# Performance work log

Measured on AMD Instinct MI355X. Metric: run time of the kernel, lower is better.

Reference implementation:

```python
import jax, jax.numpy as jnp
import numpy as np

IN_DIM, OUT_DIM = 32, 16
NUM_BINS, EMBED, HEADS = 1100, 8, 4
MN, MX = -1.0, 300.0
BATCH = 1024


def setup_inputs() -> dict:
    key = jax.random.key(0)
    ks = jax.random.split(key, 8)
    s = 1.0 / np.sqrt(EMBED)
    x = jax.random.uniform(ks[0], (BATCH, IN_DIM), jnp.float32, MN, MX)
    emb = jax.random.normal(ks[1], (IN_DIM, NUM_BINS, EMBED), jnp.float32)  # per-feature tables
    in_proj_w = jax.random.uniform(ks[2], (3 * EMBED, EMBED), jnp.float32, -s, s)
    in_proj_b = jnp.zeros((3 * EMBED,), jnp.float32)
    out_proj_w = jax.random.uniform(ks[3], (EMBED, EMBED), jnp.float32, -s, s)
    out_proj_b = jnp.zeros((EMBED,), jnp.float32)
    sl = 1.0 / np.sqrt(IN_DIM * EMBED)
    lin_w = jax.random.uniform(ks[4], (OUT_DIM, IN_DIM * EMBED), jnp.float32, -sl, sl)
    lin_b = jax.random.uniform(ks[5], (OUT_DIM,), jnp.float32, -sl, sl)
    return {"x": x, "emb": emb, "in_proj_w": in_proj_w, "in_proj_b": in_proj_b,
            "out_proj_w": out_proj_w, "out_proj_b": out_proj_b,
            "lin_w": lin_w, "lin_b": lin_b}


def reference(x, emb, in_proj_w, in_proj_b, out_proj_w, out_proj_b, lin_w, lin_b):
    B, F = x.shape
    H, hd = HEADS, EMBED // HEADS
    # clamp + bucketize (torch.bucketize right=False == searchsorted side='left')
    bins = jnp.linspace(MN, MX, NUM_BINS)
    idx = jnp.searchsorted(bins, jnp.clip(x, MN, MX), side="left")  # (B, F)
    # per-feature embedding gather
    xe = emb[jnp.arange(F)[None, :], idx]  # (B, F, E)
    # MultiheadAttention with batch_first=False: seq axis = B, batch axis = F
    Wq, Wk, Wv = jnp.split(in_proj_w, 3, axis=0)
    bq, bk, bv = jnp.split(in_proj_b, 3)
    q = (xe @ Wq.T + bq).reshape(B, F, H, hd)
    k = (xe @ Wk.T + bk).reshape(B, F, H, hd)
    v = (xe @ Wv.T + bv).reshape(B, F, H, hd)
    scores = jnp.einsum("bfhd,cfhd->fhbc", q, k) / np.sqrt(hd)  # (F, H, B, B)
    attn = jax.nn.softmax(scores, axis=-1)
    o = jnp.einsum("fhbc,cfhd->bfhd", attn, v).reshape(B, F, EMBED)
    o = o @ out_proj_w.T + out_proj_b  # (B, F, E)
    logits = o.reshape(B, F * EMBED) @ lin_w.T + lin_b  # (B, OUT_DIM)
    return jax.nn.softmax(logits, axis=-1)
```

## Files before the change

### kernel.cpp

```cpp
#include <hip/hip_runtime.h>
#include <math.h>

#define NF 32
#define NB 1100
#define NE 8
#define NH 4
#define NBATCH 1024
#define NFH 128

typedef float vf2 __attribute__((ext_vector_type(2)));

__device__ __forceinline__ float fexp2(float x){
#if __has_builtin(__builtin_amdgcn_exp2f)
  return __builtin_amdgcn_exp2f(x);
#else
  return exp2f(x);
#endif
}

__device__ __forceinline__ double bin_at(int i){
  #pragma clang fp contract(off)
  const double step = 301.0 / 1099.0;
  if (i == NB - 1) return 300.0;
  return (double)i * step + (-1.0);
}

__global__ __launch_bounds__(128) void k1_embed_qkv(
    const float* __restrict__ x, const float* __restrict__ emb,
    const float* __restrict__ W, const float* __restrict__ bias,
    float* __restrict__ q_ws, float* __restrict__ kv_ws)
{
  __shared__ float sW[192];
  __shared__ float sB[24];
  const int tid = threadIdx.x;
  for (int i = tid; i < 192; i += 128) sW[i] = W[i];
  if (tid < 24)  sB[tid] = bias[tid];
  __syncthreads();

  const int f = blockIdx.y;
  const int b = blockIdx.x * 128 + tid;

  float xv = x[b * NF + f];
  xv = fminf(fmaxf(xv, -1.0f), 300.0f);
  const double xd = (double)xv;

  int lo = 0, hi = NB;
  while (lo < hi) {
    const int mid = (lo + hi) >> 1;
    if (bin_at(mid) < xd) lo = mid + 1; else hi = mid;
  }
  const int idx = lo;

  const float4* ep = (const float4*)(emb + ((size_t)f * NB + idx) * NE);
  const float4 e0 = ep[0], e1 = ep[1];
  const float xe[8] = {e0.x, e0.y, e0.z, e0.w, e1.x, e1.y, e1.z, e1.w};

  float qv[8], kv[8], vv[8];
  #pragma unroll
  for (int i = 0; i < 8; ++i) { qv[i] = sB[i]; kv[i] = sB[8+i]; vv[i] = sB[16+i]; }
  #pragma unroll
  for (int j = 0; j < 8; ++j) {
    const float xj = xe[j];
    #pragma unroll
    for (int i = 0; i < 8; ++i) {
      qv[i] = fmaf(xj, sW[      i*8 + j], qv[i]);
      kv[i] = fmaf(xj, sW[ 64 + i*8 + j], kv[i]);
      vv[i] = fmaf(xj, sW[128 + i*8 + j], vv[i]);
    }
  }

  const float QS = (float)(1.4426950408889634 / 1.4142135623730951);
  float2* qp = (float2*)q_ws;
  float4* kvp = (float4*)kv_ws;
  #pragma unroll
  for (int h = 0; h < NH; ++h) {
    const int fh = f * NH + h;
    qp [fh * NBATCH + b] = make_float2(qv[2*h] * QS, qv[2*h+1] * QS);
    kvp[fh * NBATCH + b] = make_float4(kv[2*h], kv[2*h+1], vv[2*h], vv[2*h+1]);
  }
}

__global__ __launch_bounds__(512) void k2_attn(
    const float* __restrict__ q_ws, const float* __restrict__ kv_ws,
    float* __restrict__ o_ws)
{
  __shared__ float4 skk[512];
  __shared__ float4 svv[512];
  __shared__ float sred[8];
  __shared__ float sl[256], so0[256], so1[256];
  const int tid = threadIdx.x;
  const int fh = blockIdx.y;

  const float4* kvg = (const float4*)kv_ws + (size_t)fh * NBATCH;
  const float4 a0 = kvg[2*tid], a1 = kvg[2*tid+1];
  skk[tid] = make_float4(a0.x, a1.x, a0.y, a1.y);
  svv[tid] = make_float4(a0.z, a1.z, a0.w, a1.w);
  float mx2 = fmaxf(fmaf(a0.x, a0.x, a0.y * a0.y), fmaf(a1.x, a1.x, a1.y * a1.y));
  #pragma unroll
  for (int off = 32; off >= 1; off >>= 1)
    mx2 = fmaxf(mx2, __shfl_xor(mx2, off, 64));
  if ((tid & 63) == 0) sred[tid >> 6] = mx2;
  __syncthreads();
  float Mn2 = sred[0];
  #pragma unroll
  for (int w = 1; w < 8; ++w) Mn2 = fmaxf(Mn2, sred[w]);
  const float Mn = sqrtf(Mn2);

  const int qi = tid & 255;
  const int half = tid >> 8;
  const int b = blockIdx.x * 256 + qi;
  const float2 q = ((const float2*)q_ws)[(size_t)fh * NBATCH + b];
  const float negm = -sqrtf(fmaf(q.x, q.x, q.y * q.y)) * Mn;

  const vf2 qxx = {q.x, q.x};
  const vf2 qyy = {q.y, q.y};
  const vf2 nm2 = {negm, negm};
  vf2 lp = {0.0f, 0.0f}, o0p = {0.0f, 0.0f}, o1p = {0.0f, 0.0f};

  const int p0 = half << 8;
  #pragma unroll 8
  for (int i = 0; i < 256; ++i) {
    const float4 kk = skk[p0 + i];
    const float4 vv = svv[p0 + i];
    const vf2 k0p = {kk.x, kk.y}, k1p = {kk.z, kk.w};
    const vf2 v0p = {vv.x, vv.y}, v1p = {vv.z, vv.w};
    const vf2 s = qxx * k0p + qyy * k1p + nm2;
    vf2 pp; pp.x = fexp2(s.x); pp.y = fexp2(s.y);
    lp  += pp;
    o0p += pp * v0p;
    o1p += pp * v1p;
  }
  float l = lp.x + lp.y, o0 = o0p.x + o0p.y, o1 = o1p.x + o1p.y;

  if (half == 1) { sl[qi] = l; so0[qi] = o0; so1[qi] = o1; }
  __syncthreads();
  if (half == 0) {
    l += sl[qi]; o0 += so0[qi]; o1 += so1[qi];
    const float inv = 1.0f / l;
    ((float2*)o_ws)[(size_t)fh * NBATCH + b] = make_float2(o0 * inv, o1 * inv);
  }
}

__global__ __launch_bounds__(256) void k3_final(
    const float* __restrict__ o_ws, const float* __restrict__ opw,
    const float* __restrict__ opb,  const float* __restrict__ lw,
    const float* __restrict__ lb,   float* __restrict__ out)
{
  __shared__ float sWc[4096];
  __shared__ float sbc[16];
  __shared__ float sWo[64];
  const int tid = threadIdx.x;
  if (tid < 64) sWo[tid] = opw[tid];
  __syncthreads();
  #pragma unroll
  for (int i = tid; i < 4096; i += 256) {
    const int t = i >> 8, fe = i & 255;
    const int f8 = fe & ~7, e2 = fe & 7;
    float acc = 0.0f;
    #pragma unroll
    for (int e = 0; e < 8; ++e) acc = fmaf(lw[t*256 + f8 + e], sWo[e*8 + e2], acc);
    sWc[i] = acc;
  }
  {
    const int t = tid >> 4, seg = tid & 15;
    float acc = 0.0f;
    #pragma unroll
    for (int j = 0; j < 16; ++j) {
      const int fe = seg * 16 + j;
      acc = fmaf(lw[t*256 + fe], opb[fe & 7], acc);
    }
    #pragma unroll
    for (int off = 8; off >= 1; off >>= 1) acc += __shfl_xor(acc, off, 64);
    if (seg == 0) sbc[t] = acc + lb[t];
  }
  __syncthreads();

  const int gid = blockIdx.x * 256 + tid;
  const int b = gid >> 4;
  const int t = gid & 15;
  const float2* op = (const float2*)o_ws;
  const float2* wp = (const float2*)sWc + t * 128;
  float acc = sbc[t];
  #pragma unroll 8
  for (int fh = 0; fh < NFH; ++fh) {
    const float2 ov = op[(size_t)fh * NBATCH + b];
    const float2 wv = wp[fh];
    acc = fmaf(ov.x, wv.x, fmaf(ov.y, wv.y, acc));
  }
  float mx = acc;
  #pragma unroll
  for (int off = 8; off >= 1; off >>= 1) mx = fmaxf(mx, __shfl_xor(mx, off, 64));
  const float p = expf(acc - mx);
  float s = p;
  #pragma unroll
  for (int off = 8; off >= 1; off >>= 1) s += __shfl_xor(s, off, 64);
  out[gid] = p / s;
}

extern "C" void kernel_launch(void* const* d_in, const int* in_sizes, int n_in,
                              void* d_out, int out_size, void* d_ws, size_t ws_size,
                              hipStream_t stream)
{
  const float* x   = (const float*)d_in[0];
  const float* emb = (const float*)d_in[1];
  const float* ipw = (const float*)d_in[2];
  const float* ipb = (const float*)d_in[3];
  const float* opw = (const float*)d_in[4];
  const float* opb = (const float*)d_in[5];
  const float* lw  = (const float*)d_in[6];
  const float* lb  = (const float*)d_in[7];

  float* ws    = (float*)d_ws;
  float* q_ws  = ws;
  float* kv_ws = ws + 262144;
  float* o_ws  = ws + 786432;

  k1_embed_qkv<<<dim3(8, NF), 128, 0, stream>>>(x, emb, ipw, ipb, q_ws, kv_ws);
  k2_attn<<<dim3(4, NFH), 512, 0, stream>>>(q_ws, kv_ws, o_ws);
  k3_final<<<64, 256, 0, stream>>>(o_ws, opw, opb, lw, lb, (float*)d_out);
}
```

Measured before the change: 109.2 us.

## Fuse embedding/QKV projection into attention kernel and precompute combined output weights

Folds the bucketize, embedding gather and K/V/Q projection into the attention kernel. Each (feature, head) block recomputes K/V for all 1024 rows straight into shared memory, so the Q/KV workspace round trip and one launch go away. Folding out_proj into lin_w now happens once, in a few blocks of the attention kernel, instead of in every final-kernel block. The final kernel uses 64-thread blocks over 256 blocks. The cost is redundant work: each of the 4 query blocks per head repeats the binary search and K/V projection, and each of the 4 heads per feature repeats the gather.

```diff
diff --git a/kernel.cpp b/kernel.cpp
--- a/kernel.cpp
+++ b/kernel.cpp
@@ -25,82 +25,82 @@
   return (double)i * step + (-1.0);
 }
 
-__global__ __launch_bounds__(128) void k1_embed_qkv(
-    const float* __restrict__ x, const float* __restrict__ emb,
-    const float* __restrict__ W, const float* __restrict__ bias,
-    float* __restrict__ q_ws, float* __restrict__ kv_ws)
+__global__ __launch_bounds__(512) void k12_attn(
+    const float* __restrict__ x,   const float* __restrict__ emb,
+    const float* __restrict__ W,   const float* __restrict__ bias,
+    const float* __restrict__ opw, const float* __restrict__ opb,
+    const float* __restrict__ lw,  const float* __restrict__ lb,
+    float* __restrict__ o_ws, float* __restrict__ Wcomb, float* __restrict__ bcomb)
 {
-  __shared__ float sW[192];
-  __shared__ float sB[24];
-  const int tid = threadIdx.x;
-  for (int i = tid; i < 192; i += 128) sW[i] = W[i];
-  if (tid < 24)  sB[tid] = bias[tid];
-  __syncthreads();
-
-  const int f = blockIdx.y;
-  const int b = blockIdx.x * 128 + tid;
-
-  float xv = x[b * NF + f];
-  xv = fminf(fmaxf(xv, -1.0f), 300.0f);
-  const double xd = (double)xv;
-
-  int lo = 0, hi = NB;
-  while (lo < hi) {
-    const int mid = (lo + hi) >> 1;
-    if (bin_at(mid) < xd) lo = mid + 1; else hi = mid;
-  }
-  const int idx = lo;
-
-  const float4* ep = (const float4*)(emb + ((size_t)f * NB + idx) * NE);
-  const float4 e0 = ep[0], e1 = ep[1];
-  const float xe[8] = {e0.x, e0.y, e0.z, e0.w, e1.x, e1.y, e1.z, e1.w};
-
-  float qv[8], kv[8], vv[8];
-  #pragma unroll
-  for (int i = 0; i < 8; ++i) { qv[i] = sB[i]; kv[i] = sB[8+i]; vv[i] = sB[16+i]; }
-  #pragma unroll
-  for (int j = 0; j < 8; ++j) {
-    const float xj = xe[j];
-    #pragma unroll
-    for (int i = 0; i < 8; ++i) {
-      qv[i] = fmaf(xj, sW[      i*8 + j], qv[i]);
-      kv[i] = fmaf(xj, sW[ 64 + i*8 + j], kv[i]);
-      vv[i] = fmaf(xj, sW[128 + i*8 + j], vv[i]);
-    }
-  }
-
-  const float QS = (float)(1.4426950408889634 / 1.4142135623730951);
-  float2* qp = (float2*)q_ws;
-  float4* kvp = (float4*)kv_ws;
-  #pragma unroll
-  for (int h = 0; h < NH; ++h) {
-    const int fh = f * NH + h;
-    qp [fh * NBATCH + b] = make_float2(qv[2*h] * QS, qv[2*h+1] * QS);
-    kvp[fh * NBATCH + b] = make_float4(kv[2*h], kv[2*h+1], vv[2*h], vv[2*h+1]);
-  }
-}
-
-__global__ __launch_bounds__(512) void k2_attn(
-    const float* __restrict__ q_ws, const float* __restrict__ kv_ws,
-    float* __restrict__ o_ws)
-{
-  __shared__ float4 skk[512];
-  __shared__ float4 svv[512];
+  __shared__ float skkf[2048];
+  __shared__ float svvf[2048];
+  __shared__ float sq[512];
   __shared__ float sred[8];
   __shared__ float sl[256], so0[256], so1[256];
+  __shared__ float sWb[48];
+  __shared__ float sBb[6];
+
   const int tid = threadIdx.x;
-  const int fh = blockIdx.y;
-
-  const float4* kvg = (const float4*)kv_ws + (size_t)fh * NBATCH;
-  const float4 a0 = kvg[2*tid], a1 = kvg[2*tid+1];
-  skk[tid] = make_float4(a0.x, a1.x, a0.y, a1.y);
-  svv[tid] = make_float4(a0.z, a1.z, a0.w, a1.w);
-  float mx2 = fmaxf(fmaf(a0.x, a0.x, a0.y * a0.y), fmaf(a1.x, a1.x, a1.y * a1.y));
+  const int bq  = blockIdx.x;
+  const int fh  = blockIdx.y;
+  const int f   = fh >> 2, h = fh & 3;
+
+  if (tid < 48) {
+    const int r = tid >> 3, j = tid & 7;
+    sWb[tid] = W[((r >> 1) * 8 + 2 * h + (r & 1)) * 8 + j];
+  }
+  if (tid < 6) sBb[tid] = bias[(tid >> 1) * 8 + 2 * h + (tid & 1)];
+  __syncthreads();
+
+  const float QS = (float)(1.4426950408889634 / 1.4142135623730951);
+  const int qlo = bq << 8;
+  float mx2 = 0.0f;
+
+  #pragma unroll
+  for (int r2 = 0; r2 < 2; ++r2) {
+    const int row = tid + (r2 << 9);
+    float xv = x[row * NF + f];
+    xv = fminf(fmaxf(xv, -1.0f), 300.0f);
+    const double xd = (double)xv;
+    int lo = 0, hi = NB;
+    while (lo < hi) {
+      const int mid = (lo + hi) >> 1;
+      if (bin_at(mid) < xd) lo = mid + 1; else hi = mid;
+    }
+    const float4* ep = (const float4*)(emb + ((size_t)f * NB + lo) * NE);
+    const float4 e0 = ep[0], e1 = ep[1];
+    const float xe[8] = {e0.x, e0.y, e0.z, e0.w, e1.x, e1.y, e1.z, e1.w};
+
+    float k0 = sBb[2], k1 = sBb[3], v0 = sBb[4], v1 = sBb[5];
+    #pragma unroll
+    for (int j = 0; j < 8; ++j) {
+      k0 = fmaf(xe[j], sWb[16 + j], k0);
+      k1 = fmaf(xe[j], sWb[24 + j], k1);
+      v0 = fmaf(xe[j], sWb[32 + j], v0);
+      v1 = fmaf(xe[j], sWb[40 + j], v1);
+    }
+    const int i = row >> 1, par = row & 1;
+    skkf[4*i + par]     = k0;  skkf[4*i + 2 + par] = k1;
+    svvf[4*i + par]     = v0;  svvf[4*i + 2 + par] = v1;
+    mx2 = fmaxf(mx2, fmaf(k0, k0, k1 * k1));
+
+    const unsigned qi = (unsigned)(row - qlo);
+    if (qi < 256u) {
+      float q0 = sBb[0], q1 = sBb[1];
+      #pragma unroll
+      for (int j = 0; j < 8; ++j) {
+        q0 = fmaf(xe[j], sWb[j],     q0);
+        q1 = fmaf(xe[j], sWb[8 + j], q1);
+      }
+      sq[2*qi] = q0 * QS;  sq[2*qi + 1] = q1 * QS;
+    }
+  }
   #pragma unroll
   for (int off = 32; off >= 1; off >>= 1)
     mx2 = fmaxf(mx2, __shfl_xor(mx2, off, 64));
   if ((tid & 63) == 0) sred[tid >> 6] = mx2;
   __syncthreads();
+
   float Mn2 = sred[0];
   #pragma unroll
   for (int w = 1; w < 8; ++w) Mn2 = fmaxf(Mn2, sred[w]);
@@ -108,8 +108,7 @@
 
   const int qi = tid & 255;
   const int half = tid >> 8;
-  const int b = blockIdx.x * 256 + qi;
-  const float2 q = ((const float2*)q_ws)[(size_t)fh * NBATCH + b];
+  const float2 q = ((const float2*)sq)[qi];
   const float negm = -sqrtf(fmaf(q.x, q.x, q.y * q.y)) * Mn;
 
   const vf2 qxx = {q.x, q.x};
@@ -117,6 +116,8 @@
   const vf2 nm2 = {negm, negm};
   vf2 lp = {0.0f, 0.0f}, o0p = {0.0f, 0.0f}, o1p = {0.0f, 0.0f};
 
+  const float4* skk = (const float4*)skkf;
+  const float4* svv = (const float4*)svvf;
   const int p0 = half << 8;
   #pragma unroll 8
   for (int i = 0; i < 256; ++i) {
@@ -137,45 +138,45 @@
   if (half == 0) {
     l += sl[qi]; o0 += so0[qi]; o1 += so1[qi];
     const float inv = 1.0f / l;
+    const int b = qlo + qi;
     ((float2*)o_ws)[(size_t)fh * NBATCH + b] = make_float2(o0 * inv, o1 * inv);
   }
-}
-
-__global__ __launch_bounds__(256) void k3_final(
-    const float* __restrict__ o_ws, const float* __restrict__ opw,
-    const float* __restrict__ opb,  const float* __restrict__ lw,
-    const float* __restrict__ lb,   float* __restrict__ out)
+
+  if (bq == 0 && fh < 16) {
+    const int t = fh;
+    float bacc = 0.0f;
+    if (tid < 256) {
+      const int f8 = tid & ~7, e2 = tid & 7;
+      float wacc = 0.0f;
+      #pragma unroll
+      for (int e = 0; e < 8; ++e)
+        wacc = fmaf(lw[t*256 + f8 + e], opw[e*8 + e2], wacc);
+      Wcomb[t*256 + tid] = wacc;
+      bacc = lw[t*256 + tid] * opb[tid & 7];
+    }
+    #pragma unroll
+    for (int off = 32; off >= 1; off >>= 1) bacc += __shfl_xor(bacc, off, 64);
+    if ((tid & 63) == 0) sred[tid >> 6] = bacc;
+    __syncthreads();
+    if (tid == 0) bcomb[t] = sred[0] + sred[1] + sred[2] + sred[3] + lb[t];
+  }
+}
+
+__global__ __launch_bounds__(64) void k3_final(
+    const float* __restrict__ o_ws, const float* __restrict__ Wcomb,
+    const float* __restrict__ bcomb, float* __restrict__ out)
 {
   __shared__ float sWc[4096];
   __shared__ float sbc[16];
-  __shared__ float sWo[64];
   const int tid = threadIdx.x;
-  if (tid < 64) sWo[tid] = opw[tid];
-  __syncthreads();
-  #pragma unroll
-  for (int i = tid; i < 4096; i += 256) {
-    const int t = i >> 8, fe = i & 255;
-    const int f8 = fe & ~7, e2 = fe & 7;
-    float acc = 0.0f;
-    #pragma unroll
-    for (int e = 0; e < 8; ++e) acc = fmaf(lw[t*256 + f8 + e], sWo[e*8 + e2], acc);
-    sWc[i] = acc;
-  }
-  {
-    const int t = tid >> 4, seg = tid & 15;
-    float acc = 0.0f;
-    #pragma unroll
-    for (int j = 0; j < 16; ++j) {
-      const int fe = seg * 16 + j;
-      acc = fmaf(lw[t*256 + fe], opb[fe & 7], acc);
-    }
-    #pragma unroll
-    for (int off = 8; off >= 1; off >>= 1) acc += __shfl_xor(acc, off, 64);
-    if (seg == 0) sbc[t] = acc + lb[t];
-  }
-  __syncthreads();
-
-  const int gid = blockIdx.x * 256 + tid;
+  const float4* wg = (const float4*)Wcomb;
+  float4* ws4 = (float4*)sWc;
+  #pragma unroll
+  for (int i = tid; i < 1024; i += 64) ws4[i] = wg[i];
+  if (tid < 16) sbc[tid] = bcomb[tid];
+  __syncthreads();
+
+  const int gid = blockIdx.x * 64 + tid;
   const int b = gid >> 4;
   const int t = gid & 15;
   const float2* op = (const float2*)o_ws;
@@ -211,11 +212,11 @@
   const float* lb  = (const float*)d_in[7];
 
   float* ws    = (float*)d_ws;
-  float* q_ws  = ws;
-  float* kv_ws = ws + 262144;
-  float* o_ws  = ws + 786432;
-
-  k1_embed_qkv<<<dim3(8, NF), 128, 0, stream>>>(x, emb, ipw, ipb, q_ws, kv_ws);
-  k2_attn<<<dim3(4, NFH), 512, 0, stream>>>(q_ws, kv_ws, o_ws);
-  k3_final<<<64, 256, 0, stream>>>(o_ws, opw, opb, lw, lb, (float*)d_out);
-}
+  float* o_ws  = ws;
+  float* Wcomb = ws + 262144;
+  float* bcomb = ws + 266240;
+
+  k12_attn<<<dim3(4, NFH), 512, 0, stream>>>(x, emb, ipw, ipb, opw, opb, lw, lb,
+                                             o_ws, Wcomb, bcomb);
+  k3_final<<<256, 64, 0, stream>>>(o_ws, Wcomb, bcomb, (float*)d_out);
+}
```

Result: no change. 108.2 us (-0.9%).
